# Kernel optimization log

Hardware: AMD Instinct MI355X
Metric: run time of the kernel (lower is better)

The kernel has to match this reference:

```python
import jax, jax.numpy as jnp
import numpy as np

HIDDEN = 512
BATCH = 32
SEQ = 4096


def setup_inputs() -> dict:
    key = jax.random.key(0)
    k1, k2, k3, k4, k5 = jax.random.split(key, 5)
    s = 1.0 / np.sqrt(2 * HIDDEN)
    return {
        "hidden": jax.random.normal(k1, (BATCH, HIDDEN), dtype=jnp.float32),
        "encoder_outputs": jax.random.normal(k2, (BATCH, SEQ, HIDDEN), dtype=jnp.float32),
        "attn_w": jax.random.uniform(k3, (HIDDEN, 2 * HIDDEN), dtype=jnp.float32, minval=-s, maxval=s),
        "attn_b": jax.random.uniform(k4, (HIDDEN,), dtype=jnp.float32, minval=-s, maxval=s),
        "v_w": jax.random.uniform(k5, (1, HIDDEN), dtype=jnp.float32, minval=-1.0 / np.sqrt(HIDDEN), maxval=1.0 / np.sqrt(HIDDEN)),
    }


def reference(hidden, encoder_outputs, attn_w, attn_b, v_w):
    # attn_w maps concat([hidden_repeated, encoder_outputs]) of size 2H -> H.
    # Split into the hidden part and encoder part to avoid materializing the concat.
    H = hidden.shape[-1]
    Wh = attn_w[:, :H]   # [H, H] applied to repeated hidden
    We = attn_w[:, H:]   # [H, H] applied to encoder outputs
    # hidden contribution is constant over seq_len: [B, 1, H]
    h_proj = jnp.einsum("bh,kh->bk", hidden, Wh)[:, None, :] + attn_b
    e_proj = jnp.einsum("bsh,kh->bsk", encoder_outputs, We)
    energy = jnp.tanh(h_proj + e_proj)                       # [B, S, H]
    scores = jnp.einsum("bsk,k->bs", energy, v_w[0])          # [B, S]
    return jax.nn.softmax(scores, axis=1)
```

## Files before the change

### kernel.cpp

```cpp
#include <hip/hip_runtime.h>

#define HIDDEN 512
#define SEQN 4096
#define BM 128
#define BK 64

typedef __attribute__((ext_vector_type(8))) short short8;
typedef __attribute__((ext_vector_type(4))) float f32x4;

__device__ __forceinline__ unsigned cvtpk(float a, float b) {
  unsigned r;
  asm("v_cvt_pk_bf16_f32 %0, %1, %2" : "=v"(r) : "v"(a), "v"(b));
  return r;
}

__global__ void k_convW(const float* __restrict__ attn_w, short* __restrict__ wbf) {
  int i = blockIdx.x * 256 + threadIdx.x;
  int f = i * 4;
  int k = f >> 9;
  int h = f & 511;
  const float4 v = *reinterpret_cast<const float4*>(attn_w + k * 1024 + 512 + h);
  uint2 o = { cvtpk(v.x, v.y), cvtpk(v.z, v.w) };
  *reinterpret_cast<uint2*>(wbf + f) = o;
}

__global__ void k_hproj(const float* __restrict__ hidden, const float* __restrict__ attn_w,
                        const float* __restrict__ attn_b, float* __restrict__ hp) {
  int b = blockIdx.y;
  int k = blockIdx.x * 128 + threadIdx.x;
  __shared__ float hsh[HIDDEN];
  *reinterpret_cast<float4*>(hsh + threadIdx.x * 4) =
      *reinterpret_cast<const float4*>(hidden + b * HIDDEN + threadIdx.x * 4);
  __syncthreads();
  const float* wr = attn_w + k * 1024;
  float4 s4 = {0.f, 0.f, 0.f, 0.f};
  #pragma unroll 8
  for (int h = 0; h < HIDDEN; h += 4) {
    float4 wv = *reinterpret_cast<const float4*>(wr + h);
    s4.x += wv.x * hsh[h];
    s4.y += wv.y * hsh[h + 1];
    s4.z += wv.z * hsh[h + 2];
    s4.w += wv.w * hsh[h + 3];
  }
  hp[b * HIDDEN + k] = attn_b[k] + ((s4.x + s4.y) + (s4.z + s4.w));
}

__global__ __launch_bounds__(512, 2) void k_main(
    const float* __restrict__ enc, const short* __restrict__ wbf,
    const float* __restrict__ hp, const float* __restrict__ vw,
    float* __restrict__ scores) {
  __shared__ __align__(16) short A_ls[2][BM * BK];
  __shared__ float part[8][BM];

  const int tid = threadIdx.x;
  const int w = tid >> 6;
  const int l = tid & 63;
  const int lq = l >> 4;
  const int lr = l & 15;

  const int bid = blockIdx.x;
  const int b = bid >> 5;
  const int s0 = (bid & 31) * BM;
  const float* encB = enc + ((size_t)b * SEQN + s0) * HIDDEN;

  const int r0 = tid >> 3;
  const int cg = tid & 7;
  const int wa0 = r0 * 64 + ((cg * 8) ^ ((r0 & 7) << 3));
  const int wa1 = (r0 + 64) * 64 + ((cg * 8) ^ ((r0 & 7) << 3));

  const short* wBase = wbf + (w * 64 + lr) * HIDDEN + lq * 8;

  f32x4 acc[8][4];
  #pragma unroll
  for (int mi = 0; mi < 8; ++mi)
    #pragma unroll
    for (int ni = 0; ni < 4; ++ni)
      acc[mi][ni] = (f32x4){0.f, 0.f, 0.f, 0.f};

  float4 ga0, ga1, gb0, gb1;
  {
    const float* p0 = encB + r0 * HIDDEN + cg * 8;
    const float* p1 = p0 + 64 * HIDDEN;
    ga0 = *reinterpret_cast<const float4*>(p0);
    ga1 = *reinterpret_cast<const float4*>(p0 + 4);
    gb0 = *reinterpret_cast<const float4*>(p1);
    gb1 = *reinterpret_cast<const float4*>(p1 + 4);
  }
  {
    uint4 u0 = { cvtpk(ga0.x, ga0.y), cvtpk(ga0.z, ga0.w), cvtpk(ga1.x, ga1.y), cvtpk(ga1.z, ga1.w) };
    uint4 u1 = { cvtpk(gb0.x, gb0.y), cvtpk(gb0.z, gb0.w), cvtpk(gb1.x, gb1.y), cvtpk(gb1.z, gb1.w) };
    *reinterpret_cast<uint4*>(&A_ls[0][wa0]) = u0;
    *reinterpret_cast<uint4*>(&A_ls[0][wa1]) = u1;
  }
  __syncthreads();

  #pragma unroll 1
  for (int st = 0; st < 8; ++st) {
    const int cur = st & 1;
    if (st < 7) {
      const float* p0 = encB + r0 * HIDDEN + (st + 1) * BK + cg * 8;
      const float* p1 = p0 + 64 * HIDDEN;
      ga0 = *reinterpret_cast<const float4*>(p0);
      ga1 = *reinterpret_cast<const float4*>(p0 + 4);
      gb0 = *reinterpret_cast<const float4*>(p1);
      gb1 = *reinterpret_cast<const float4*>(p1 + 4);
    }
    short8 wf0[4], wf1[4];
    #pragma unroll
    for (int ni = 0; ni < 4; ++ni)
      wf0[ni] = *reinterpret_cast<const short8*>(wBase + ni * (16 * HIDDEN) + st * BK);
    #pragma unroll
    for (int ni = 0; ni < 4; ++ni)
      wf1[ni] = *reinterpret_cast<const short8*>(wBase + ni * (16 * HIDDEN) + st * BK + 32);

    {
      short8 af[8];
      #pragma unroll
      for (int mi = 0; mi < 8; ++mi)
        af[mi] = *reinterpret_cast<const short8*>(
            &A_ls[cur][(mi * 16 + lr) * 64 + ((lq * 8) ^ ((lr & 7) << 3))]);
      #pragma unroll
      for (int mi = 0; mi < 8; ++mi)
        #pragma unroll
        for (int ni = 0; ni < 4; ++ni)
          acc[mi][ni] = __builtin_amdgcn_mfma_f32_16x16x32_bf16(af[mi], wf0[ni], acc[mi][ni], 0, 0, 0);
    }
    {
      short8 af[8];
      #pragma unroll
      for (int mi = 0; mi < 8; ++mi)
        af[mi] = *reinterpret_cast<const short8*>(
            &A_ls[cur][(mi * 16 + lr) * 64 + ((32 + lq * 8) ^ ((lr & 7) << 3))]);
      #pragma unroll
      for (int mi = 0; mi < 8; ++mi)
        #pragma unroll
        for (int ni = 0; ni < 4; ++ni)
          acc[mi][ni] = __builtin_amdgcn_mfma_f32_16x16x32_bf16(af[mi], wf1[ni], acc[mi][ni], 0, 0, 0);
    }
    if (st < 7) {
      uint4 u0 = { cvtpk(ga0.x, ga0.y), cvtpk(ga0.z, ga0.w), cvtpk(ga1.x, ga1.y), cvtpk(ga1.z, ga1.w) };
      uint4 u1 = { cvtpk(gb0.x, gb0.y), cvtpk(gb0.z, gb0.w), cvtpk(gb1.x, gb1.y), cvtpk(gb1.z, gb1.w) };
      *reinterpret_cast<uint4*>(&A_ls[cur ^ 1][wa0]) = u0;
      *reinterpret_cast<uint4*>(&A_ls[cur ^ 1][wa1]) = u1;
    }
    __syncthreads();
  }

  float hpv[4], vv[4];
  {
    const float* hpb = hp + b * HIDDEN;
    const int colb = w * 64 + lr;
    #pragma unroll
    for (int ni = 0; ni < 4; ++ni) {
      hpv[ni] = hpb[colb + ni * 16];
      vv[ni]  = vw[colb + ni * 16];
    }
  }
  float rp[8][4];
  #pragma unroll
  for (int mi = 0; mi < 8; ++mi)
    #pragma unroll
    for (int r = 0; r < 4; ++r) {
      float s = 0.f;
      #pragma unroll
      for (int ni = 0; ni < 4; ++ni) {
        float x = acc[mi][ni][r] + hpv[ni];
        float e = __expf(2.0f * x);
        float th = 1.0f - 2.0f / (e + 1.0f);
        s += th * vv[ni];
      }
      rp[mi][r] = s;
    }
  #pragma unroll
  for (int mk = 1; mk <= 8; mk <<= 1)
    #pragma unroll
    for (int mi = 0; mi < 8; ++mi)
      #pragma unroll
      for (int r = 0; r < 4; ++r)
        rp[mi][r] += __shfl_xor(rp[mi][r], mk, 64);
  if (lr == 0) {
    #pragma unroll
    for (int mi = 0; mi < 8; ++mi)
      #pragma unroll
      for (int r = 0; r < 4; ++r)
        part[w][mi * 16 + lq * 4 + r] = rp[mi][r];
  }
  __syncthreads();
  if (tid < BM) {
    float s = 0.f;
    #pragma unroll
    for (int ww = 0; ww < 8; ++ww) s += part[ww][tid];
    scores[b * SEQN + s0 + tid] = s;
  }
}

__global__ void k_softmax(const float* __restrict__ scores, float* __restrict__ out) {
  const int b = blockIdx.x;
  const int t = threadIdx.x;
  const float* row = scores + b * SEQN;
  float4 x[4];
  #pragma unroll
  for (int i = 0; i < 4; ++i)
    x[i] = *reinterpret_cast<const float4*>(row + (i * 256 + t) * 4);
  float m = -1e30f;
  #pragma unroll
  for (int i = 0; i < 4; ++i)
    m = fmaxf(m, fmaxf(fmaxf(x[i].x, x[i].y), fmaxf(x[i].z, x[i].w)));
  #pragma unroll
  for (int mk = 1; mk < 64; mk <<= 1) m = fmaxf(m, __shfl_xor(m, mk, 64));
  __shared__ float redmax[4], redsum[4];
  if ((t & 63) == 0) redmax[t >> 6] = m;
  __syncthreads();
  m = fmaxf(fmaxf(redmax[0], redmax[1]), fmaxf(redmax[2], redmax[3]));
  float sum = 0.f;
  #pragma unroll
  for (int i = 0; i < 4; ++i) {
    x[i].x = __expf(x[i].x - m); sum += x[i].x;
    x[i].y = __expf(x[i].y - m); sum += x[i].y;
    x[i].z = __expf(x[i].z - m); sum += x[i].z;
    x[i].w = __expf(x[i].w - m); sum += x[i].w;
  }
  #pragma unroll
  for (int mk = 1; mk < 64; mk <<= 1) sum += __shfl_xor(sum, mk, 64);
  if ((t & 63) == 0) redsum[t >> 6] = sum;
  __syncthreads();
  sum = redsum[0] + redsum[1] + redsum[2] + redsum[3];
  float inv = 1.0f / sum;
  #pragma unroll
  for (int i = 0; i < 4; ++i) {
    float4 o = { x[i].x * inv, x[i].y * inv, x[i].z * inv, x[i].w * inv };
    *reinterpret_cast<float4*>(out + b * SEQN + (i * 256 + t) * 4) = o;
  }
}

extern "C" void kernel_launch(void* const* d_in, const int* in_sizes, int n_in,
                              void* d_out, int out_size, void* d_ws, size_t ws_size,
                              hipStream_t stream) {
  const float* hidden = (const float*)d_in[0];
  const float* enc    = (const float*)d_in[1];
  const float* attn_w = (const float*)d_in[2];
  const float* attn_b = (const float*)d_in[3];
  const float* vw     = (const float*)d_in[4];
  float* out = (float*)d_out;

  short* wbf    = (short*)d_ws;
  float* hp     = (float*)((char*)d_ws + 512 * 1024);
  float* scores = (float*)((char*)d_ws + 512 * 1024 + 64 * 1024);

  k_convW<<<256, 256, 0, stream>>>(attn_w, wbf);
  k_hproj<<<dim3(4, 32), 128, 0, stream>>>(hidden, attn_w, attn_b, hp);
  k_main<<<1024, 512, 0, stream>>>(enc, wbf, hp, vw, scores);
  k_softmax<<<32, 256, 0, stream>>>(scores, out);
}
```

Baseline: 456.4 us.

## Shrink main tile to 64 rows with 4 waves each covering 128 columns

The main GEMM block now handles 64 sequence rows with 256 threads instead of 128 rows with 512 threads. Each wave covers 128 output columns and 4 row fragments, so the grid doubles to 2048 blocks. The point is more blocks in flight and less LDS per block, which could help latency hiding on a memory-bound encoder stream. The cost is that each block reloads the full bf16 weight matrix for half as many rows, doubling weight traffic from L2, and more B-fragment registers per wave may lower occupancy.

```diff
diff --git a/kernel.cpp b/kernel.cpp
--- a/kernel.cpp
+++ b/kernel.cpp
@@ -2,7 +2,7 @@
 
 #define HIDDEN 512
 #define SEQN 4096
-#define BM 128
+#define BM 64
 #define BK 64
 
 typedef __attribute__((ext_vector_type(8))) short short8;
@@ -45,12 +45,12 @@
   hp[b * HIDDEN + k] = attn_b[k] + ((s4.x + s4.y) + (s4.z + s4.w));
 }
 
-__global__ __launch_bounds__(512, 2) void k_main(
+__global__ __launch_bounds__(256, 2) void k_main(
     const float* __restrict__ enc, const short* __restrict__ wbf,
     const float* __restrict__ hp, const float* __restrict__ vw,
     float* __restrict__ scores) {
   __shared__ __align__(16) short A_ls[2][BM * BK];
-  __shared__ float part[8][BM];
+  __shared__ float part[4][BM];
 
   const int tid = threadIdx.x;
   const int w = tid >> 6;
@@ -59,36 +59,36 @@
   const int lr = l & 15;
 
   const int bid = blockIdx.x;
-  const int b = bid >> 5;
-  const int s0 = (bid & 31) * BM;
+  const int b = bid >> 6;
+  const int s0 = (bid & 63) * BM;
   const float* encB = enc + ((size_t)b * SEQN + s0) * HIDDEN;
 
-  const int r0 = tid >> 3;
-  const int cg = tid & 7;
-  const int wa0 = r0 * 64 + ((cg * 8) ^ ((r0 & 7) << 3));
-  const int wa1 = (r0 + 64) * 64 + ((cg * 8) ^ ((r0 & 7) << 3));
-
-  const short* wBase = wbf + (w * 64 + lr) * HIDDEN + lq * 8;
-
-  f32x4 acc[8][4];
-  #pragma unroll
-  for (int mi = 0; mi < 8; ++mi)
-    #pragma unroll
-    for (int ni = 0; ni < 4; ++ni)
+  const int r0 = tid >> 2;
+  const int cg = tid & 3;
+  const int swz = (r0 & 7) << 3;
+  const int wa0 = r0 * 64 + ((cg * 16) ^ swz);
+  const int wa1 = r0 * 64 + ((cg * 16 + 8) ^ swz);
+
+  const short* wBase = wbf + (w * 128 + lr) * HIDDEN + lq * 8;
+
+  f32x4 acc[4][8];
+  #pragma unroll
+  for (int mi = 0; mi < 4; ++mi)
+    #pragma unroll
+    for (int ni = 0; ni < 8; ++ni)
       acc[mi][ni] = (f32x4){0.f, 0.f, 0.f, 0.f};
 
-  float4 ga0, ga1, gb0, gb1;
+  float4 ga0, ga1, ga2, ga3;
   {
-    const float* p0 = encB + r0 * HIDDEN + cg * 8;
-    const float* p1 = p0 + 64 * HIDDEN;
-    ga0 = *reinterpret_cast<const float4*>(p0);
-    ga1 = *reinterpret_cast<const float4*>(p0 + 4);
-    gb0 = *reinterpret_cast<const float4*>(p1);
-    gb1 = *reinterpret_cast<const float4*>(p1 + 4);
+    const float* p = encB + r0 * HIDDEN + cg * 16;
+    ga0 = *reinterpret_cast<const float4*>(p);
+    ga1 = *reinterpret_cast<const float4*>(p + 4);
+    ga2 = *reinterpret_cast<const float4*>(p + 8);
+    ga3 = *reinterpret_cast<const float4*>(p + 12);
   }
   {
     uint4 u0 = { cvtpk(ga0.x, ga0.y), cvtpk(ga0.z, ga0.w), cvtpk(ga1.x, ga1.y), cvtpk(ga1.z, ga1.w) };
-    uint4 u1 = { cvtpk(gb0.x, gb0.y), cvtpk(gb0.z, gb0.w), cvtpk(gb1.x, gb1.y), cvtpk(gb1.z, gb1.w) };
+    uint4 u1 = { cvtpk(ga2.x, ga2.y), cvtpk(ga2.z, ga2.w), cvtpk(ga3.x, ga3.y), cvtpk(ga3.z, ga3.w) };
     *reinterpret_cast<uint4*>(&A_ls[0][wa0]) = u0;
     *reinterpret_cast<uint4*>(&A_ls[0][wa1]) = u1;
   }
@@ -98,72 +98,71 @@
   for (int st = 0; st < 8; ++st) {
     const int cur = st & 1;
     if (st < 7) {
-      const float* p0 = encB + r0 * HIDDEN + (st + 1) * BK + cg * 8;
-      const float* p1 = p0 + 64 * HIDDEN;
-      ga0 = *reinterpret_cast<const float4*>(p0);
-      ga1 = *reinterpret_cast<const float4*>(p0 + 4);
-      gb0 = *reinterpret_cast<const float4*>(p1);
-      gb1 = *reinterpret_cast<const float4*>(p1 + 4);
-    }
-    short8 wf0[4], wf1[4];
-    #pragma unroll
-    for (int ni = 0; ni < 4; ++ni)
+      const float* p = encB + r0 * HIDDEN + (st + 1) * BK + cg * 16;
+      ga0 = *reinterpret_cast<const float4*>(p);
+      ga1 = *reinterpret_cast<const float4*>(p + 4);
+      ga2 = *reinterpret_cast<const float4*>(p + 8);
+      ga3 = *reinterpret_cast<const float4*>(p + 12);
+    }
+    short8 wf0[8], wf1[8];
+    #pragma unroll
+    for (int ni = 0; ni < 8; ++ni)
       wf0[ni] = *reinterpret_cast<const short8*>(wBase + ni * (16 * HIDDEN) + st * BK);
     #pragma unroll
-    for (int ni = 0; ni < 4; ++ni)
+    for (int ni = 0; ni < 8; ++ni)
       wf1[ni] = *reinterpret_cast<const short8*>(wBase + ni * (16 * HIDDEN) + st * BK + 32);
 
     {
-      short8 af[8];
-      #pragma unroll
-      for (int mi = 0; mi < 8; ++mi)
+      short8 af[4];
+      #pragma unroll
+      for (int mi = 0; mi < 4; ++mi)
         af[mi] = *reinterpret_cast<const short8*>(
             &A_ls[cur][(mi * 16 + lr) * 64 + ((lq * 8) ^ ((lr & 7) << 3))]);
       #pragma unroll
-      for (int mi = 0; mi < 8; ++mi)
+      for (int mi = 0; mi < 4; ++mi)
         #pragma unroll
-        for (int ni = 0; ni < 4; ++ni)
+        for (int ni = 0; ni < 8; ++ni)
           acc[mi][ni] = __builtin_amdgcn_mfma_f32_16x16x32_bf16(af[mi], wf0[ni], acc[mi][ni], 0, 0, 0);
     }
     {
-      short8 af[8];
-      #pragma unroll
-      for (int mi = 0; mi < 8; ++mi)
+      short8 af[4];
+      #pragma unroll
+      for (int mi = 0; mi < 4; ++mi)
         af[mi] = *reinterpret_cast<const short8*>(
             &A_ls[cur][(mi * 16 + lr) * 64 + ((32 + lq * 8) ^ ((lr & 7) << 3))]);
       #pragma unroll
-      for (int mi = 0; mi < 8; ++mi)
+      for (int mi = 0; mi < 4; ++mi)
         #pragma unroll
-        for (int ni = 0; ni < 4; ++ni)
+        for (int ni = 0; ni < 8; ++ni)
           acc[mi][ni] = __builtin_amdgcn_mfma_f32_16x16x32_bf16(af[mi], wf1[ni], acc[mi][ni], 0, 0, 0);
     }
     if (st < 7) {
       uint4 u0 = { cvtpk(ga0.x, ga0.y), cvtpk(ga0.z, ga0.w), cvtpk(ga1.x, ga1.y), cvtpk(ga1.z, ga1.w) };
-      uint4 u1 = { cvtpk(gb0.x, gb0.y), cvtpk(gb0.z, gb0.w), cvtpk(gb1.x, gb1.y), cvtpk(gb1.z, gb1.w) };
+      uint4 u1 = { cvtpk(ga2.x, ga2.y), cvtpk(ga2.z, ga2.w), cvtpk(ga3.x, ga3.y), cvtpk(ga3.z, ga3.w) };
       *reinterpret_cast<uint4*>(&A_ls[cur ^ 1][wa0]) = u0;
       *reinterpret_cast<uint4*>(&A_ls[cur ^ 1][wa1]) = u1;
     }
     __syncthreads();
   }
 
-  float hpv[4], vv[4];
+  float hpv[8], vv[8];
   {
     const float* hpb = hp + b * HIDDEN;
-    const int colb = w * 64 + lr;
-    #pragma unroll
-    for (int ni = 0; ni < 4; ++ni) {
+    const int colb = w * 128 + lr;
+    #pragma unroll
+    for (int ni = 0; ni < 8; ++ni) {
       hpv[ni] = hpb[colb + ni * 16];
       vv[ni]  = vw[colb + ni * 16];
     }
   }
-  float rp[8][4];
-  #pragma unroll
-  for (int mi = 0; mi < 8; ++mi)
+  float rp[4][4];
+  #pragma unroll
+  for (int mi = 0; mi < 4; ++mi)
     #pragma unroll
     for (int r = 0; r < 4; ++r) {
       float s = 0.f;
       #pragma unroll
-      for (int ni = 0; ni < 4; ++ni) {
+      for (int ni = 0; ni < 8; ++ni) {
         float x = acc[mi][ni][r] + hpv[ni];
         float e = __expf(2.0f * x);
         float th = 1.0f - 2.0f / (e + 1.0f);
@@ -174,22 +173,20 @@
   #pragma unroll
   for (int mk = 1; mk <= 8; mk <<= 1)
     #pragma unroll
-    for (int mi = 0; mi < 8; ++mi)
+    for (int mi = 0; mi < 4; ++mi)
       #pragma unroll
       for (int r = 0; r < 4; ++r)
         rp[mi][r] += __shfl_xor(rp[mi][r], mk, 64);
   if (lr == 0) {
     #pragma unroll
-    for (int mi = 0; mi < 8; ++mi)
+    for (int mi = 0; mi < 4; ++mi)
       #pragma unroll
       for (int r = 0; r < 4; ++r)
         part[w][mi * 16 + lq * 4 + r] = rp[mi][r];
   }
   __syncthreads();
   if (tid < BM) {
-    float s = 0.f;
-    #pragma unroll
-    for (int ww = 0; ww < 8; ++ww) s += part[ww][tid];
+    float s = part[0][tid] + part[1][tid] + part[2][tid] + part[3][tid];
     scores[b * SEQN + s0 + tid] = s;
   }
 }
@@ -249,6 +246,6 @@
 
   k_convW<<<256, 256, 0, stream>>>(attn_w, wbf);
   k_hproj<<<dim3(4, 32), 128, 0, stream>>>(hidden, attn_w, attn_b, hp);
-  k_main<<<1024, 512, 0, stream>>>(enc, wbf, hp, vw, scores);
+  k_main<<<2048, 256, 0, stream>>>(enc, wbf, hp, vw, scores);
   k_softmax<<<32, 256, 0, stream>>>(scores, out);
 }
```

Result: slower. 476.6 us (+4.4%).
